# Kernel optimization log

Measured on AMD Instinct MI355X. Metric: run time of the kernel, lower is better.

## Reference

```python
import jax, jax.numpy as jnp
import numpy as np

L, C, D = 8, 8192, 128          # levels, classes per level, type_embedding_dim
P, F, K, S, NF = 8, 4, 4, 4, 16384
NBASIC = 11
N = L * C


def setup_inputs() -> dict:
    rng = np.random.default_rng(0)
    key = jax.random.key(0)
    ks = jax.random.split(key, 12)

    def lvl_idx(shape):
        # class at level l may only reference classes with id < l*C (topological DAG)
        return jnp.asarray(np.stack([rng.integers(0, l * C, size=shape) for l in range(1, L)]), jnp.int32)

    s = 1.0 / np.sqrt(D)

    def gru_w(k):
        return jax.random.normal(k, (D, 3 * D), jnp.float32) * s

    inp = {
        'basic_ids': jnp.asarray(rng.integers(0, NBASIC, size=(C,)), jnp.int32),
        'prop_idx': lvl_idx((C, P)),
        'func_param_idx': lvl_idx((C, F, K)),
        'func_ret_idx': lvl_idx((C, F)),
        'super_idx': lvl_idx((C, S)),
        'glob_param_idx': jnp.asarray(rng.integers(0, N, size=(NF, K)), jnp.int32),
        'glob_ret_idx': jnp.asarray(rng.integers(0, N, size=(NF,)), jnp.int32),
        'basic_emb': jax.random.normal(ks[0], (NBASIC, D), jnp.float32) * 0.05,
        'empty_params': jax.random.normal(ks[1], (D,), jnp.float32) * 0.05,
        'empty_members': jax.random.normal(ks[2], (D,), jnp.float32) * 0.05,
        'W_fn': jax.random.normal(ks[3], (2 * D, D), jnp.float32) * s,
        'pW': gru_w(ks[4]), 'pU': gru_w(ks[5]), 'pb': jnp.zeros((2, 3 * D), jnp.float32),
        'mW': gru_w(ks[6]), 'mU': gru_w(ks[7]), 'mb': jnp.zeros((2, 3 * D), jnp.float32),
        'sW': gru_w(ks[8]), 'sU': gru_w(ks[9]), 'sb': jnp.zeros((2, 3 * D), jnp.float32),
    }
    return inp


def gru_run(xs, W, U, b):
    """Keras GRU (reset_after=True). xs: [B,T,D] -> final hidden [B,D]."""
    bi, br = b[0], b[1]
    gx = jnp.einsum('btd,de->bte', xs, W) + bi  # input projections, all steps at once

    def step(h, g):
        gh = h @ U + br
        xz, xr, xn = jnp.split(g, 3, axis=-1)
        hz, hr, hn = jnp.split(gh, 3, axis=-1)
        z = jax.nn.sigmoid(xz + hz)
        r = jax.nn.sigmoid(xr + hr)
        n = jnp.tanh(xn + r * hn)
        return z * h + (1.0 - z) * n, None

    h0 = jnp.zeros((xs.shape[0], W.shape[0]), xs.dtype)
    h, _ = jax.lax.scan(step, h0, jnp.swapaxes(gx, 0, 1))
    return h


def fn_embed(param_idx, ret_idx, table, empty_params, W_fn, pW, pU, pb):
    """get_embedding_for_function, batched. param_idx: [..., K]; ret_idx: [...]."""
    lead = param_idx.shape[:-1]
    n = int(np.prod(lead))
    pe = table[param_idx].reshape(n, K, D)                       # gather param embeddings
    seq = jnp.concatenate([jnp.broadcast_to(empty_params, (n, 1, D)), pe], axis=1)
    h = gru_run(seq, pW, pU, pb)                                 # [n, D]
    ret = table[ret_idx].reshape(n, D)
    out = jnp.concatenate([h, ret], axis=-1) @ W_fn              # [n, D]
    return out.reshape(lead + (D,))


def reference(basic_ids, prop_idx, func_param_idx, func_ret_idx, super_idx,
              glob_param_idx, glob_ret_idx, basic_emb, empty_params, empty_members,
              W_fn, pW, pU, pb, mW, mU, mb, sW, sU, sb):
    table = jnp.zeros((N, D), basic_emb.dtype)
    table = table.at[:C].set(basic_emb[basic_ids])               # level 0: basic types

    member_fns = []
    for l in range(1, L):                                        # topological levels
        fn_e = fn_embed(func_param_idx[l - 1], func_ret_idx[l - 1], table,
                        empty_params, W_fn, pW, pU, pb)          # [C, F, D]
        member_fns.append(fn_e)
        props = table[prop_idx[l - 1]]                           # [C, P, D]
        mseq = jnp.concatenate([jnp.broadcast_to(empty_members, (C, 1, D)), props, fn_e], axis=1)
        m = gru_run(mseq, mW, mU, mb)                            # [C, D]
        sseq = jnp.concatenate([table[super_idx[l - 1]], m[:, None, :]], axis=1)
        e = gru_run(sseq, sW, sU, sb)                            # [C, D]
        table = table.at[l * C:(l + 1) * C].set(e)

    glob = fn_embed(glob_param_idx, glob_ret_idx, table, empty_params, W_fn, pW, pU, pb)
    member_fn = jnp.stack(member_fns)                            # [L-1, C, F, D]
    return table, glob, member_fn
```

## Files before the change

kernel.cpp:

```cpp
#include <hip/hip_runtime.h>

#define LVL 8
#define C 8192
#define D 128
#define P 8
#define F 4
#define K 4
#define S 4
#define NF 16384
#define NTOT (LVL*C)

typedef __bf16 bf16;
typedef bf16 bf16x4 __attribute__((ext_vector_type(4)));
typedef bf16 bf16x8 __attribute__((ext_vector_type(8)));
typedef float f32x4 __attribute__((ext_vector_type(4)));

__device__ __forceinline__ f32x4 mfma16(bf16x8 a, bf16x8 b, f32x4 c) {
  return __builtin_amdgcn_mfma_f32_16x16x32_bf16(a, b, c, 0, 0, 0);
}
__device__ __forceinline__ bf16x4 b4(f32x4 v) {
  bf16x4 r; r[0]=(bf16)v[0]; r[1]=(bf16)v[1]; r[2]=(bf16)v[2]; r[3]=(bf16)v[3]; return r;
}
__device__ __forceinline__ float sigm(float x) { return __builtin_amdgcn_rcpf(1.f + __expf(-x)); }
__device__ __forceinline__ float tanh_(float x) { return 1.f - 2.f*__builtin_amdgcn_rcpf(1.f + __expf(2.f*x)); }

__device__ __forceinline__ void bar() {
  asm volatile("s_waitcnt lgkmcnt(0)\n\ts_barrier" ::: "memory");
}

__device__ __forceinline__ float ldf(const void* b, long i, int f) {
  return f ? ((const float*)b)[i] : (float)((const bf16*)b)[i];
}
__device__ __forceinline__ bf16x8 ldx8(const void* b, long i, int f) {
  if (f) {
    f32x4 a = *(const f32x4*)((const float*)b + i);
    f32x4 c = *(const f32x4*)((const float*)b + i + 4);
    bf16x8 r;
    r[0]=(bf16)a[0]; r[1]=(bf16)a[1]; r[2]=(bf16)a[2]; r[3]=(bf16)a[3];
    r[4]=(bf16)c[0]; r[5]=(bf16)c[1]; r[6]=(bf16)c[2]; r[7]=(bf16)c[3];
    return r;
  }
  return *(const bf16x8*)((const bf16*)b + i);
}
__device__ __forceinline__ f32x4 ld4f(const void* b, long i, int f) {
  if (f) return *(const f32x4*)((const float*)b + i);
  bf16x4 t = *(const bf16x4*)((const bf16*)b + i);
  f32x4 r; r[0]=(float)t[0]; r[1]=(float)t[1]; r[2]=(float)t[2]; r[3]=(float)t[3]; return r;
}
__device__ __forceinline__ void st4(void* b, long i, int f, f32x4 v) {
  if (f) *(f32x4*)((float*)b + i) = v;
  else   *(bf16x4*)((bf16*)b + i) = b4(v);
}

template<int NT, bool SKIPU>
__device__ __forceinline__ void gru_step(
    const bf16x8 (&AU)[3][4], const bf16x8 (&AW)[3][4],
    const f32x4& zb, const f32x4& rb, const f32x4& nbx, const f32x4& nbh,
    const bf16 (* __restrict__ hbuf)[136], const bf16 (* __restrict__ xbuf)[136],
    int l15, int quad, int gc,
    f32x4 (&h)[NT], bf16 (*hout)[136])
{
  f32x4 aZ[NT], aR[NT], aNx[NT], aNh[NT];
#pragma unroll
  for (int nt = 0; nt < NT; nt++) { aZ[nt]=zb; aR[nt]=rb; aNx[nt]=nbx; aNh[nt]=nbh; }
#pragma unroll
  for (int kt = 0; kt < 4; kt++) {
    bf16x8 Bh[NT], Bx[NT];
#pragma unroll
    for (int nt = 0; nt < NT; nt++) {
      if (!SKIPU) Bh[nt] = *(const bf16x8*)&hbuf[nt*16 + l15][kt*32 + quad*8];
      Bx[nt] = *(const bf16x8*)&xbuf[nt*16 + l15][kt*32 + quad*8];
    }
#pragma unroll
    for (int nt = 0; nt < NT; nt++) {
      if (!SKIPU) aZ[nt]  = mfma16(AU[0][kt], Bh[nt], aZ[nt]);
      aZ[nt]  = mfma16(AW[0][kt], Bx[nt], aZ[nt]);
      if (!SKIPU) aR[nt]  = mfma16(AU[1][kt], Bh[nt], aR[nt]);
      aR[nt]  = mfma16(AW[1][kt], Bx[nt], aR[nt]);
      if (!SKIPU) aNh[nt] = mfma16(AU[2][kt], Bh[nt], aNh[nt]);
      aNx[nt] = mfma16(AW[2][kt], Bx[nt], aNx[nt]);
    }
  }
#pragma unroll
  for (int nt = 0; nt < NT; nt++) {
    f32x4 hn = h[nt];
#pragma unroll
    for (int i = 0; i < 4; i++) {
      float z = sigm(aZ[nt][i]);
      float r = sigm(aR[nt][i]);
      float n = tanh_(aNx[nt][i] + r*aNh[nt][i]);
      hn[i] = z*hn[i] + (1.f - z)*n;
    }
    h[nt] = hn;
    *(bf16x4*)&hout[nt*16 + l15][gc] = b4(hn);
  }
}

__global__ __launch_bounds__(512, 1) void level_kernel(
    const bf16* __restrict__ pUt, const bf16* __restrict__ pWt, const float* __restrict__ b2p,
    const bf16* __restrict__ wtT,
    const bf16* __restrict__ mUt, const bf16* __restrict__ mWt, const float* __restrict__ b2m,
    const bf16* __restrict__ sUt, const bf16* __restrict__ sWt, const float* __restrict__ b2s,
    const void* __restrict__ empty_params, const void* __restrict__ empty_members,
    const void* __restrict__ tabR, int tabRf,
    const int* __restrict__ fpi, const int* __restrict__ fri,
    const int* __restrict__ ppi, const int* __restrict__ spi,
    void* __restrict__ out, long memfnEB, long tabEB,
    bf16* __restrict__ shadowW,
    const int* __restrict__ flagp, int mode)
{
  __shared__ __align__(16) bf16 hT[2][32][136];
  __shared__ __align__(16) bf16 xT[2][32][136];
  __shared__ __align__(16) bf16 feT[4][32][136];

  const int isf32 = *flagp;
  const int rf = (tabRf < 0) ? isf32 : tabRf;
  const int tid = threadIdx.x;
  const int w = tid >> 6;
  const int l15 = tid & 15;
  const int quad = (tid & 63) >> 4;
  const int gc = w*16 + quad*4;
  const int prow = tid >> 4;
  const int pc8 = (tid & 15) * 8;
  const int c0 = blockIdx.x * 32;

  bf16x8 AU[3][4], AW[3][4];
  f32x4 zb, rb, nbx, nbh;
  auto loadWB = [&](const bf16* Ut, const bf16* Wt, const float* b2) {
#pragma unroll
    for (int tr = 0; tr < 3; tr++)
#pragma unroll
      for (int kt = 0; kt < 4; kt++) {
        size_t o = (size_t)(tr*128 + w*16 + l15)*128 + kt*32 + quad*8;
        AU[tr][kt] = *(const bf16x8*)&Ut[o];
        AW[tr][kt] = *(const bf16x8*)&Wt[o];
      }
    zb  = *(const f32x4*)&b2[0*128 + gc];
    rb  = *(const f32x4*)&b2[1*128 + gc];
    nbx = *(const f32x4*)&b2[2*128 + gc];
    nbh = *(const f32x4*)&b2[3*128 + gc];
  };

  f32x4 hm[2];

  loadWB(pUt, pWt, b2p);
  bf16x8 eP = ldx8(empty_params, pc8, isf32);

  auto fnpass = [&](long s, int4 piv, int riv, int p) {
    bf16x8 pend0 = ldx8(tabR, (long)piv.x*128 + pc8, rf);
    bf16x8 retv  = ldx8(tabR, (long)riv*128 + pc8, rf);
    *(bf16x8*)&xT[0][prow][pc8] = eP;
    bar();

    f32x4 h[2];
#pragma unroll
    for (int nt = 0; nt < 2; nt++) { h[nt][0]=0.f; h[nt][1]=0.f; h[nt][2]=0.f; h[nt][3]=0.f; }
    bf16x8 pend1;
    int buf = 0;
#pragma unroll
    for (int t = 0; t < 5; t++) {
      if (t < 3) {
        int rn = (t==0) ? piv.y : (t==1) ? piv.z : piv.w;
        pend1 = ldx8(tabR, (long)rn*128 + pc8, rf);
      }
      if (t == 0)
        gru_step<2,true >(AU, AW, zb, rb, nbx, nbh,
                          (const bf16(*)[136])hT[buf], (const bf16(*)[136])xT[0],
                          l15, quad, gc, h, hT[1-buf]);
      else
        gru_step<2,false>(AU, AW, zb, rb, nbx, nbh,
                          (const bf16(*)[136])hT[buf], (const bf16(*)[136])xT[t&1],
                          l15, quad, gc, h, hT[1-buf]);
      if (t < 4) { *(bf16x8*)&xT[(t+1)&1][prow][pc8] = pend0; pend0 = pend1; }
      bar();
      buf ^= 1;
    }
    *(bf16x8*)&xT[0][prow][pc8] = retv;
    bar();

    f32x4 acc[2];
#pragma unroll
    for (int nt = 0; nt < 2; nt++) { acc[nt][0]=0.f; acc[nt][1]=0.f; acc[nt][2]=0.f; acc[nt][3]=0.f; }
#pragma unroll
    for (int kt = 0; kt < 8; kt++) {
      bf16x8 A = *(const bf16x8*)&wtT[(size_t)(w*16 + l15)*256 + kt*32 + quad*8];
#pragma unroll
      for (int nt = 0; nt < 2; nt++) {
        bf16x8 B = (kt < 4) ? *(const bf16x8*)&hT[buf][nt*16 + l15][kt*32 + quad*8]
                            : *(const bf16x8*)&xT[0][nt*16 + l15][(kt-4)*32 + quad*8];
        acc[nt] = mfma16(A, B, acc[nt]);
      }
    }
#pragma unroll
    for (int nt = 0; nt < 2; nt++) {
      long so = mode ? ((long)blockIdx.x*32 + nt*16 + l15)
                     : ((long)(c0 + nt*16 + l15)*4 + p);
      st4(out, memfnEB + so*128 + gc, isf32, acc[nt]);
      if (!mode) *(bf16x4*)&feT[p][nt*16 + l15][gc] = b4(acc[nt]);
    }
    bar();
  };

  if (mode) {
    long s = (long)blockIdx.x*32 + prow;
    int4 p0 = *(const int4*)&fpi[s*4];
    int r0 = fri[s];
    fnpass(s, p0, r0, 0);
    return;
  }
  {
    long sB = (long)(c0 + prow)*4;
    int4 p0 = *(const int4*)&fpi[(sB+0)*4];
    int4 p1 = *(const int4*)&fpi[(sB+1)*4];
    int4 p2 = *(const int4*)&fpi[(sB+2)*4];
    int4 p3 = *(const int4*)&fpi[(sB+3)*4];
    int4 rr = *(const int4*)&fri[sB];
    fnpass(sB+0, p0, rr.x, 0);
    fnpass(sB+1, p1, rr.y, 1);
    fnpass(sB+2, p2, rr.z, 2);
    fnpass(sB+3, p3, rr.w, 3);
  }

  loadWB(mUt, mWt, b2m);
  int4 ma  = *(const int4*)&ppi[(size_t)(c0 + prow)*8];
  int4 mb2 = *(const int4*)&ppi[(size_t)(c0 + prow)*8 + 4];
  bf16x8 pendB0 = ldx8(tabR, (long)ma.x*128 + pc8, rf);
  bf16x8 eM = ldx8(empty_members, pc8, isf32);
  *(bf16x8*)&xT[0][prow][pc8] = eM;
  bar();

#pragma unroll
  for (int nt = 0; nt < 2; nt++) { hm[nt][0]=0.f; hm[nt][1]=0.f; hm[nt][2]=0.f; hm[nt][3]=0.f; }
  {
    bf16x8 pendB1;
    int buf = 0;
#pragma unroll
    for (int t = 0; t < 13; t++) {
      if (t < 7) {
        int rn = (t==0)?ma.y:(t==1)?ma.z:(t==2)?ma.w:(t==3)?mb2.x:(t==4)?mb2.y:(t==5)?mb2.z:mb2.w;
        pendB1 = ldx8(tabR, (long)rn*128 + pc8, rf);
      }
      const bf16 (*xb)[136] = (t < 9) ? (const bf16(*)[136])xT[t&1]
                                      : (const bf16(*)[136])feT[t-9];
      if (t == 0)
        gru_step<2,true >(AU, AW, zb, rb, nbx, nbh,
                          (const bf16(*)[136])hT[buf], xb, l15, quad, gc, hm, hT[1-buf]);
      else
        gru_step<2,false>(AU, AW, zb, rb, nbx, nbh,
                          (const bf16(*)[136])hT[buf], xb, l15, quad, gc, hm, hT[1-buf]);
      if (t < 8) { *(bf16x8*)&xT[(t+1)&1][prow][pc8] = pendB0; pendB0 = pendB1; }
      bar();
      buf ^= 1;
    }
  }

  loadWB(sUt, sWt, b2s);
  int4 sa = *(const int4*)&spi[(size_t)(c0 + prow)*4];
  bf16x8 x0v    = ldx8(tabR, (long)sa.x*128 + pc8, rf);
  bf16x8 pendC0 = ldx8(tabR, (long)sa.y*128 + pc8, rf);
  *(bf16x8*)&xT[0][prow][pc8] = x0v;
  bar();

  f32x4 hs[2];
#pragma unroll
  for (int nt = 0; nt < 2; nt++) { hs[nt][0]=0.f; hs[nt][1]=0.f; hs[nt][2]=0.f; hs[nt][3]=0.f; }
  {
    bf16x8 pendC1;
    int buf = 0;
#pragma unroll
    for (int t = 0; t < 5; t++) {
      if (t < 2) {
        int rn = (t==0) ? sa.z : sa.w;
        pendC1 = ldx8(tabR, (long)rn*128 + pc8, rf);
      }
      if (t == 0)
        gru_step<2,true >(AU, AW, zb, rb, nbx, nbh,
                          (const bf16(*)[136])hT[buf], (const bf16(*)[136])xT[0],
                          l15, quad, gc, hs, hT[1-buf]);
      else
        gru_step<2,false>(AU, AW, zb, rb, nbx, nbh,
                          (const bf16(*)[136])hT[buf], (const bf16(*)[136])xT[t&1],
                          l15, quad, gc, hs, hT[1-buf]);
      if (t < 3) { *(bf16x8*)&xT[(t+1)&1][prow][pc8] = pendC0; pendC0 = pendC1; }
      else if (t == 3) {
#pragma unroll
        for (int nt = 0; nt < 2; nt++) *(bf16x4*)&xT[0][nt*16 + l15][gc] = b4(hm[nt]);
      }
      bar();
      buf ^= 1;
    }
  }
#pragma unroll
  for (int nt = 0; nt < 2; nt++) {
    long row = (long)(c0 + nt*16 + l15);
    st4(out, tabEB + row*128 + gc, isf32, hs[nt]);
    if (shadowW) *(bf16x4*)&shadowW[row*128 + gc] = b4(hs[nt]);
  }
}

__global__ void detect_kernel(const void* be, int* flag) {
  if (threadIdx.x == 0 && blockIdx.x == 0) {
    const unsigned short* u = (const unsigned short*)be;
    int f = 0;
    for (int i = 0; i < 128; i++) {
      unsigned e = (u[i] >> 7) & 0xFF;
      if (e >= 128) f = 1;
    }
    *flag = f;
  }
}

__global__ void convert_kernel(const void* pW, const void* pU, const void* mW, const void* mU,
                               const void* sW, const void* sU, const void* W_fn,
                               const void* pb, const void* mb, const void* sb,
                               bf16* pWt, bf16* pUt, bf16* mWt, bf16* mUt,
                               bf16* sWt, bf16* sUt, bf16* wtT,
                               float* b2p, float* b2m, float* b2s,
                               const int* flagp) {
  const int f = *flagp;
  int i = blockIdx.x*256 + threadIdx.x;
  const int TT = 384*128;
  if (i < 6*TT) {
    int which = i / TT, j = i - which*TT;
    int c = j >> 7, k = j & 127;
    const void* src = (which==0)?pW:(which==1)?pU:(which==2)?mW:(which==3)?mU:(which==4)?sW:sU;
    bf16* dst = (which==0)?pWt:(which==1)?pUt:(which==2)?mWt:(which==3)?mUt:(which==4)?sWt:sUt;
    dst[c*128 + k] = (bf16)ldf(src, (long)k*384 + c, f);
    return;
  }
  i -= 6*TT;
  if (i < 128*256) { int c = i >> 8, k = i & 255; wtT[c*256 + k] = (bf16)ldf(W_fn, (long)k*128 + c, f); return; }
  i -= 128*256;
  if (i < 3*512) {
    int which = i >> 9, j = i & 511;
    const void* b = (which==0)?pb:(which==1)?mb:sb;
    float* dst = (which==0)?b2p:(which==1)?b2m:b2s;
    int g = j >> 7, cc = j & 127;
    float v;
    if (g == 0)      v = ldf(b, cc, f)       + ldf(b, 384 + cc, f);
    else if (g == 1) v = ldf(b, 128 + cc, f) + ldf(b, 512 + cc, f);
    else if (g == 2) v = ldf(b, 256 + cc, f);
    else             v = ldf(b, 640 + cc, f);
    dst[j] = v;
  }
}

__global__ void level0_kernel(const int* __restrict__ basic_ids, const void* basic_emb,
                              void* out, bf16* __restrict__ shadow,
                              const int* __restrict__ flagp) {
  const int f = *flagp;
  int i = blockIdx.x*256 + threadIdx.x;
  int row = i >> 5, c4 = (i & 31) * 4;
  f32x4 v = ld4f(basic_emb, (long)basic_ids[row]*128 + c4, f);
  st4(out, (long)row*128 + c4, f, v);
  if (shadow) *(bf16x4*)&shadow[(long)row*128 + c4] = b4(v);
}

extern "C" void kernel_launch(void* const* d_in, const int* in_sizes, int n_in,
                              void* d_out, int out_size, void* d_ws, size_t ws_size,
                              hipStream_t stream) {
  const int* basic_ids      = (const int*)d_in[0];
  const int* prop_idx       = (const int*)d_in[1];
  const int* func_param_idx = (const int*)d_in[2];
  const int* func_ret_idx   = (const int*)d_in[3];
  const int* super_idx      = (const int*)d_in[4];
  const int* glob_param_idx = (const int*)d_in[5];
  const int* glob_ret_idx   = (const int*)d_in[6];
  const void* basic_emb     = d_in[7];
  const void* empty_params  = d_in[8];
  const void* empty_members = d_in[9];
  const void* W_fn = d_in[10];
  const void* pW = d_in[11]; const void* pU = d_in[12]; const void* pb = d_in[13];
  const void* mW = d_in[14]; const void* mU = d_in[15]; const void* mb = d_in[16];
  const void* sW = d_in[17]; const void* sU = d_in[18]; const void* sb = d_in[19];

  const long GB = (long)NTOT*128;
  const long MB0 = GB + (long)NF*128;
  auto FEB = [&](int l) { return MB0 + (long)(l-1)*C*F*128; };

  char* wp = (char*)d_ws;
  auto carve = [&](size_t bytes) { char* p = wp; wp += (bytes + 255) & ~(size_t)255; return p; };
  int*  flag = (int*)carve(256);
  bf16* pWt = (bf16*)carve(384*128*2);
  bf16* pUt = (bf16*)carve(384*128*2);
  bf16* mWt = (bf16*)carve(384*128*2);
  bf16* mUt = (bf16*)carve(384*128*2);
  bf16* sWt = (bf16*)carve(384*128*2);
  bf16* sUt = (bf16*)carve(384*128*2);
  bf16* wtT = (bf16*)carve(128*256*2);
  float* b2p = (float*)carve(512*4);
  float* b2m = (float*)carve(512*4);
  float* b2s = (float*)carve(512*4);
  bf16* shadow = (bf16*)carve((size_t)NTOT*128*2);

  const bool useShadow = ((size_t)(wp - (char*)d_ws) <= ws_size);
  const void* tabR = useShadow ? (const void*)shadow : (const void*)d_out;
  const int tabRf  = useShadow ? 0 : -1;
  bf16* shadowL0   = useShadow ? shadow : (bf16*)nullptr;

  detect_kernel<<<1, 64, 0, stream>>>(basic_emb, flag);
  {
    int total = 6*384*128 + 128*256 + 3*512;
    convert_kernel<<<(total + 255)/256, 256, 0, stream>>>(pW, pU, mW, mU, sW, sU, W_fn,
                                                          pb, mb, sb,
                                                          pWt, pUt, mWt, mUt, sWt, sUt, wtT,
                                                          b2p, b2m, b2s, flag);
  }
  level0_kernel<<<(C*32)/256, 256, 0, stream>>>(basic_ids, basic_emb, d_out, shadowL0, flag);

  for (int l = 1; l < LVL; l++) {
    level_kernel<<<C/32, 512, 0, stream>>>(
        pUt, pWt, b2p, wtT, mUt, mWt, b2m, sUt, sWt, b2s,
        empty_params, empty_members,
        tabR, tabRf,
        func_param_idx + (size_t)(l-1)*C*F*K,
        func_ret_idx   + (size_t)(l-1)*C*F,
        prop_idx       + (size_t)(l-1)*C*P,
        super_idx      + (size_t)(l-1)*C*S,
        d_out, FEB(l), (long)l*C*128,
        useShadow ? shadow + (size_t)l*C*128 : (bf16*)nullptr,
        flag, 0);
  }

  level_kernel<<<NF/32, 512, 0, stream>>>(
      pUt, pWt, b2p, wtT, mUt, mWt, b2m, sUt, sWt, b2s,
      empty_params, empty_members,
      tabR, tabRf,
      glob_param_idx, glob_ret_idx, nullptr, nullptr,
      d_out, GB, 0, (bf16*)nullptr,
      flag, 1);
}
```

Measured before the change: 781.6 us.

## Interleave two independent function-param GRU sequences per block to hide latency

The function-embedding GRU pass now processes two independent sequences (A and B) together in each step, using separate shared-memory h/x buffers. This halves the number of serial steps and barriers, and gives the scheduler independent MFMA and elementwise work to overlap. The return-type row loads are folded into the prefetch pipeline. The global pass now covers 64 rows per block and launches half as many blocks. In exchange, register pressure and LDS use both go up, and the global launch has fewer blocks, which lowers parallelism.

Result: slower. 808.6 us (+3.5%).

```diff
diff --git a/kernel.cpp b/kernel.cpp
--- a/kernel.cpp
+++ b/kernel.cpp
@@ -52,27 +52,26 @@
   else   *(bf16x4*)((bf16*)b + i) = b4(v);
 }
 
-template<int NT, bool SKIPU>
-__device__ __forceinline__ void gru_step(
+template<bool SKIPU>
+__device__ __forceinline__ void gru_mm(
     const bf16x8 (&AU)[3][4], const bf16x8 (&AW)[3][4],
     const f32x4& zb, const f32x4& rb, const f32x4& nbx, const f32x4& nbh,
     const bf16 (* __restrict__ hbuf)[136], const bf16 (* __restrict__ xbuf)[136],
-    int l15, int quad, int gc,
-    f32x4 (&h)[NT], bf16 (*hout)[136])
+    int l15, int quad,
+    f32x4 (&aZ)[2], f32x4 (&aR)[2], f32x4 (&aNx)[2], f32x4 (&aNh)[2])
 {
-  f32x4 aZ[NT], aR[NT], aNx[NT], aNh[NT];
-#pragma unroll
-  for (int nt = 0; nt < NT; nt++) { aZ[nt]=zb; aR[nt]=rb; aNx[nt]=nbx; aNh[nt]=nbh; }
+#pragma unroll
+  for (int nt = 0; nt < 2; nt++) { aZ[nt]=zb; aR[nt]=rb; aNx[nt]=nbx; aNh[nt]=nbh; }
 #pragma unroll
   for (int kt = 0; kt < 4; kt++) {
-    bf16x8 Bh[NT], Bx[NT];
-#pragma unroll
-    for (int nt = 0; nt < NT; nt++) {
+    bf16x8 Bh[2], Bx[2];
+#pragma unroll
+    for (int nt = 0; nt < 2; nt++) {
       if (!SKIPU) Bh[nt] = *(const bf16x8*)&hbuf[nt*16 + l15][kt*32 + quad*8];
       Bx[nt] = *(const bf16x8*)&xbuf[nt*16 + l15][kt*32 + quad*8];
     }
 #pragma unroll
-    for (int nt = 0; nt < NT; nt++) {
+    for (int nt = 0; nt < 2; nt++) {
       if (!SKIPU) aZ[nt]  = mfma16(AU[0][kt], Bh[nt], aZ[nt]);
       aZ[nt]  = mfma16(AW[0][kt], Bx[nt], aZ[nt]);
       if (!SKIPU) aR[nt]  = mfma16(AU[1][kt], Bh[nt], aR[nt]);
@@ -81,8 +80,14 @@
       aNx[nt] = mfma16(AW[2][kt], Bx[nt], aNx[nt]);
     }
   }
-#pragma unroll
-  for (int nt = 0; nt < NT; nt++) {
+}
+
+__device__ __forceinline__ void gru_elem(
+    const f32x4 (&aZ)[2], const f32x4 (&aR)[2], const f32x4 (&aNx)[2], const f32x4 (&aNh)[2],
+    int l15, int gc, f32x4 (&h)[2], bf16 (*hout)[136])
+{
+#pragma unroll
+  for (int nt = 0; nt < 2; nt++) {
     f32x4 hn = h[nt];
 #pragma unroll
     for (int i = 0; i < 4; i++) {
@@ -109,8 +114,10 @@
     bf16* __restrict__ shadowW,
     const int* __restrict__ flagp, int mode)
 {
-  __shared__ __align__(16) bf16 hT[2][32][136];
-  __shared__ __align__(16) bf16 xT[2][32][136];
+  __shared__ __align__(16) bf16 hTa[2][32][136];
+  __shared__ __align__(16) bf16 xTa[2][32][136];
+  __shared__ __align__(16) bf16 hTb[2][32][136];
+  __shared__ __align__(16) bf16 xTb[2][32][136];
   __shared__ __align__(16) bf16 feT[4][32][136];
 
   const int isf32 = *flagp;
@@ -146,79 +153,111 @@
   loadWB(pUt, pWt, b2p);
   bf16x8 eP = ldx8(empty_params, pc8, isf32);
 
-  auto fnpass = [&](long s, int4 piv, int riv, int p) {
-    bf16x8 pend0 = ldx8(tabR, (long)piv.x*128 + pc8, rf);
-    bf16x8 retv  = ldx8(tabR, (long)riv*128 + pc8, rf);
-    *(bf16x8*)&xT[0][prow][pc8] = eP;
+  auto fnpair = [&](int4 pivA, int4 pivB, int rivA, int rivB, int pa, int pb) {
+    bf16x8 pA0 = ldx8(tabR, (long)pivA.x*128 + pc8, rf);
+    bf16x8 pB0 = ldx8(tabR, (long)pivB.x*128 + pc8, rf);
+    *(bf16x8*)&xTa[0][prow][pc8] = eP;
+    *(bf16x8*)&xTb[0][prow][pc8] = eP;
     bar();
 
-    f32x4 h[2];
-#pragma unroll
-    for (int nt = 0; nt < 2; nt++) { h[nt][0]=0.f; h[nt][1]=0.f; h[nt][2]=0.f; h[nt][3]=0.f; }
-    bf16x8 pend1;
+    f32x4 hA[2], hB[2];
+#pragma unroll
+    for (int nt = 0; nt < 2; nt++) {
+      hA[nt][0]=0.f; hA[nt][1]=0.f; hA[nt][2]=0.f; hA[nt][3]=0.f;
+      hB[nt][0]=0.f; hB[nt][1]=0.f; hB[nt][2]=0.f; hB[nt][3]=0.f;
+    }
+    bf16x8 pA1, pB1;
     int buf = 0;
 #pragma unroll
     for (int t = 0; t < 5; t++) {
       if (t < 3) {
-        int rn = (t==0) ? piv.y : (t==1) ? piv.z : piv.w;
-        pend1 = ldx8(tabR, (long)rn*128 + pc8, rf);
-      }
-      if (t == 0)
-        gru_step<2,true >(AU, AW, zb, rb, nbx, nbh,
-                          (const bf16(*)[136])hT[buf], (const bf16(*)[136])xT[0],
-                          l15, quad, gc, h, hT[1-buf]);
-      else
-        gru_step<2,false>(AU, AW, zb, rb, nbx, nbh,
-                          (const bf16(*)[136])hT[buf], (const bf16(*)[136])xT[t&1],
-                          l15, quad, gc, h, hT[1-buf]);
-      if (t < 4) { *(bf16x8*)&xT[(t+1)&1][prow][pc8] = pend0; pend0 = pend1; }
+        int rnA = (t==0) ? pivA.y : (t==1) ? pivA.z : pivA.w;
+        int rnB = (t==0) ? pivB.y : (t==1) ? pivB.z : pivB.w;
+        pA1 = ldx8(tabR, (long)rnA*128 + pc8, rf);
+        pB1 = ldx8(tabR, (long)rnB*128 + pc8, rf);
+      } else if (t == 3) {
+        pA1 = ldx8(tabR, (long)rivA*128 + pc8, rf);
+        pB1 = ldx8(tabR, (long)rivB*128 + pc8, rf);
+      }
+      f32x4 aZA[2], aRA[2], aNxA[2], aNhA[2];
+      f32x4 aZB[2], aRB[2], aNxB[2], aNhB[2];
+      if (t == 0) {
+        gru_mm<true >(AU,AW,zb,rb,nbx,nbh,(const bf16(*)[136])hTa[buf],(const bf16(*)[136])xTa[0],l15,quad,aZA,aRA,aNxA,aNhA);
+        gru_mm<true >(AU,AW,zb,rb,nbx,nbh,(const bf16(*)[136])hTb[buf],(const bf16(*)[136])xTb[0],l15,quad,aZB,aRB,aNxB,aNhB);
+      } else {
+        gru_mm<false>(AU,AW,zb,rb,nbx,nbh,(const bf16(*)[136])hTa[buf],(const bf16(*)[136])xTa[t&1],l15,quad,aZA,aRA,aNxA,aNhA);
+        gru_mm<false>(AU,AW,zb,rb,nbx,nbh,(const bf16(*)[136])hTb[buf],(const bf16(*)[136])xTb[t&1],l15,quad,aZB,aRB,aNxB,aNhB);
+      }
+      gru_elem(aZA,aRA,aNxA,aNhA,l15,gc,hA,hTa[1-buf]);
+      gru_elem(aZB,aRB,aNxB,aNhB,l15,gc,hB,hTb[1-buf]);
+      if (t < 4) {
+        *(bf16x8*)&xTa[(t+1)&1][prow][pc8] = pA0; pA0 = pA1;
+        *(bf16x8*)&xTb[(t+1)&1][prow][pc8] = pB0; pB0 = pB1;
+      }
       bar();
       buf ^= 1;
     }
-    *(bf16x8*)&xT[0][prow][pc8] = retv;
+    *(bf16x8*)&xTa[0][prow][pc8] = pA0;
+    *(bf16x8*)&xTb[0][prow][pc8] = pB0;
     bar();
 
-    f32x4 acc[2];
-#pragma unroll
-    for (int nt = 0; nt < 2; nt++) { acc[nt][0]=0.f; acc[nt][1]=0.f; acc[nt][2]=0.f; acc[nt][3]=0.f; }
+    f32x4 accA[2], accB[2];
+#pragma unroll
+    for (int nt = 0; nt < 2; nt++) {
+      accA[nt][0]=0.f; accA[nt][1]=0.f; accA[nt][2]=0.f; accA[nt][3]=0.f;
+      accB[nt][0]=0.f; accB[nt][1]=0.f; accB[nt][2]=0.f; accB[nt][3]=0.f;
+    }
 #pragma unroll
     for (int kt = 0; kt < 8; kt++) {
       bf16x8 A = *(const bf16x8*)&wtT[(size_t)(w*16 + l15)*256 + kt*32 + quad*8];
 #pragma unroll
       for (int nt = 0; nt < 2; nt++) {
-        bf16x8 B = (kt < 4) ? *(const bf16x8*)&hT[buf][nt*16 + l15][kt*32 + quad*8]
-                            : *(const bf16x8*)&xT[0][nt*16 + l15][(kt-4)*32 + quad*8];
-        acc[nt] = mfma16(A, B, acc[nt]);
+        bf16x8 Ba = (kt < 4) ? *(const bf16x8*)&hTa[buf][nt*16 + l15][kt*32 + quad*8]
+                             : *(const bf16x8*)&xTa[0][nt*16 + l15][(kt-4)*32 + quad*8];
+        accA[nt] = mfma16(A, Ba, accA[nt]);
+        bf16x8 Bb = (kt < 4) ? *(const bf16x8*)&hTb[buf][nt*16 + l15][kt*32 + quad*8]
+                             : *(const bf16x8*)&xTb[0][nt*16 + l15][(kt-4)*32 + quad*8];
+        accB[nt] = mfma16(A, Bb, accB[nt]);
       }
     }
 #pragma unroll
     for (int nt = 0; nt < 2; nt++) {
-      long so = mode ? ((long)blockIdx.x*32 + nt*16 + l15)
-                     : ((long)(c0 + nt*16 + l15)*4 + p);
-      st4(out, memfnEB + so*128 + gc, isf32, acc[nt]);
-      if (!mode) *(bf16x4*)&feT[p][nt*16 + l15][gc] = b4(acc[nt]);
+      long soA = mode ? ((long)blockIdx.x*64 + pa*32 + nt*16 + l15)
+                      : ((long)(c0 + nt*16 + l15)*4 + pa);
+      long soB = mode ? ((long)blockIdx.x*64 + pb*32 + nt*16 + l15)
+                      : ((long)(c0 + nt*16 + l15)*4 + pb);
+      st4(out, memfnEB + soA*128 + gc, isf32, accA[nt]);
+      st4(out, memfnEB + soB*128 + gc, isf32, accB[nt]);
+      if (!mode) {
+        *(bf16x4*)&feT[pa][nt*16 + l15][gc] = b4(accA[nt]);
+        *(bf16x4*)&feT[pb][nt*16 + l15][gc] = b4(accB[nt]);
+      }
     }
     bar();
   };
 
   if (mode) {
-    long s = (long)blockIdx.x*32 + prow;
-    int4 p0 = *(const int4*)&fpi[s*4];
-    int r0 = fri[s];
-    fnpass(s, p0, r0, 0);
+    long sA = (long)blockIdx.x*64 + prow;
+    long sB = sA + 32;
+    int4 pA = *(const int4*)&fpi[sA*4];
+    int4 pB = *(const int4*)&fpi[sB*4];
+    fnpair(pA, pB, fri[sA], fri[sB], 0, 1);
     return;
   }
   {
-    long sB = (long)(c0 + prow)*4;
-    int4 p0 = *(const int4*)&fpi[(sB+0)*4];
-    int4 p1 = *(const int4*)&fpi[(sB+1)*4];
-    int4 p2 = *(const int4*)&fpi[(sB+2)*4];
-    int4 p3 = *(const int4*)&fpi[(sB+3)*4];
-    int4 rr = *(const int4*)&fri[sB];
-    fnpass(sB+0, p0, rr.x, 0);
-    fnpass(sB+1, p1, rr.y, 1);
-    fnpass(sB+2, p2, rr.z, 2);
-    fnpass(sB+3, p3, rr.w, 3);
+    long s4 = (long)(c0 + prow)*4;
+    {
+      int4 p0 = *(const int4*)&fpi[(s4+0)*4];
+      int4 p1 = *(const int4*)&fpi[(s4+1)*4];
+      int4 rr = *(const int4*)&fri[s4];
+      fnpair(p0, p1, rr.x, rr.y, 0, 1);
+    }
+    {
+      int4 p2 = *(const int4*)&fpi[(s4+2)*4];
+      int4 p3 = *(const int4*)&fpi[(s4+3)*4];
+      int4 rr = *(const int4*)&fri[s4];
+      fnpair(p2, p3, rr.z, rr.w, 2, 3);
+    }
   }
 
   loadWB(mUt, mWt, b2m);
@@ -226,7 +265,7 @@
   int4 mb2 = *(const int4*)&ppi[(size_t)(c0 + prow)*8 + 4];
   bf16x8 pendB0 = ldx8(tabR, (long)ma.x*128 + pc8, rf);
   bf16x8 eM = ldx8(empty_members, pc8, isf32);
-  *(bf16x8*)&xT[0][prow][pc8] = eM;
+  *(bf16x8*)&xTa[0][prow][pc8] = eM;
   bar();
 
 #pragma unroll
@@ -240,15 +279,15 @@
         int rn = (t==0)?ma.y:(t==1)?ma.z:(t==2)?ma.w:(t==3)?mb2.x:(t==4)?mb2.y:(t==5)?mb2.z:mb2.w;
         pendB1 = ldx8(tabR, (long)rn*128 + pc8, rf);
       }
-      const bf16 (*xb)[136] = (t < 9) ? (const bf16(*)[136])xT[t&1]
+      const bf16 (*xb)[136] = (t < 9) ? (const bf16(*)[136])xTa[t&1]
                                       : (const bf16(*)[136])feT[t-9];
+      f32x4 aZ[2], aR[2], aNx[2], aNh[2];
       if (t == 0)
-        gru_step<2,true >(AU, AW, zb, rb, nbx, nbh,
-                          (const bf16(*)[136])hT[buf], xb, l15, quad, gc, hm, hT[1-buf]);
+        gru_mm<true >(AU,AW,zb,rb,nbx,nbh,(const bf16(*)[136])hTa[buf],xb,l15,quad,aZ,aR,aNx,aNh);
       else
-        gru_step<2,false>(AU, AW, zb, rb, nbx, nbh,
-                          (const bf16(*)[136])hT[buf], xb, l15, quad, gc, hm, hT[1-buf]);
-      if (t < 8) { *(bf16x8*)&xT[(t+1)&1][prow][pc8] = pendB0; pendB0 = pendB1; }
+        gru_mm<false>(AU,AW,zb,rb,nbx,nbh,(const bf16(*)[136])hTa[buf],xb,l15,quad,aZ,aR,aNx,aNh);
+      gru_elem(aZ,aR,aNx,aNh,l15,gc,hm,hTa[1-buf]);
+      if (t < 8) { *(bf16x8*)&xTa[(t+1)&1][prow][pc8] = pendB0; pendB0 = pendB1; }
       bar();
       buf ^= 1;
     }
@@ -258,7 +297,7 @@
   int4 sa = *(const int4*)&spi[(size_t)(c0 + prow)*4];
   bf16x8 x0v    = ldx8(tabR, (long)sa.x*128 + pc8, rf);
   bf16x8 pendC0 = ldx8(tabR, (long)sa.y*128 + pc8, rf);
-  *(bf16x8*)&xT[0][prow][pc8] = x0v;
+  *(bf16x8*)&xTa[0][prow][pc8] = x0v;
   bar();
 
   f32x4 hs[2];
@@ -273,18 +312,16 @@
         int rn = (t==0) ? sa.z : sa.w;
         pendC1 = ldx8(tabR, (long)rn*128 + pc8, rf);
       }
+      f32x4 aZ[2], aR[2], aNx[2], aNh[2];
       if (t == 0)
-        gru_step<2,true >(AU, AW, zb, rb, nbx, nbh,
-                          (const bf16(*)[136])hT[buf], (const bf16(*)[136])xT[0],
-                          l15, quad, gc, hs, hT[1-buf]);
+        gru_mm<true >(AU,AW,zb,rb,nbx,nbh,(const bf16(*)[136])hTa[buf],(const bf16(*)[136])xTa[0],l15,quad,aZ,aR,aNx,aNh);
       else
-        gru_step<2,false>(AU, AW, zb, rb, nbx, nbh,
-                          (const bf16(*)[136])hT[buf], (const bf16(*)[136])xT[t&1],
-                          l15, quad, gc, hs, hT[1-buf]);
-      if (t < 3) { *(bf16x8*)&xT[(t+1)&1][prow][pc8] = pendC0; pendC0 = pendC1; }
+        gru_mm<false>(AU,AW,zb,rb,nbx,nbh,(const bf16(*)[136])hTa[buf],(const bf16(*)[136])xTa[t&1],l15,quad,aZ,aR,aNx,aNh);
+      gru_elem(aZ,aR,aNx,aNh,l15,gc,hs,hTa[1-buf]);
+      if (t < 3) { *(bf16x8*)&xTa[(t+1)&1][prow][pc8] = pendC0; pendC0 = pendC1; }
       else if (t == 3) {
 #pragma unroll
-        for (int nt = 0; nt < 2; nt++) *(bf16x4*)&xT[0][nt*16 + l15][gc] = b4(hm[nt]);
+        for (int nt = 0; nt < 2; nt++) *(bf16x4*)&xTa[0][nt*16 + l15][gc] = b4(hm[nt]);
       }
       bar();
       buf ^= 1;
@@ -422,7 +459,7 @@
         flag, 0);
   }
 
-  level_kernel<<<NF/32, 512, 0, stream>>>(
+  level_kernel<<<NF/64, 512, 0, stream>>>(
       pUt, pWt, b2p, wtT, mUt, mWt, b2m, sUt, sWt, b2s,
       empty_params, empty_members,
       tabR, tabRf,
```

## Template level kernel on rows per block, shrink to 16 rows for occupancy

Applied to the files above, without the earlier changes.

The level kernel is templated on the number of classes per block (16 or 32). At runtime it picks 16 when the occupancy query reports at least two resident blocks per CU. Launch bounds rise from one to four blocks per CU, and gate biases move from registers into shared memory to cut register pressure. Gather loads shrink to 4-element vectors, and index loads move inside each pass. The aim is more concurrent blocks to hide gather and barrier latency, at the cost of fewer MFMA tiles per weight load and possible register spilling under the tighter bound.

After: 2.013 ms. +157.5%, slower.

```diff
diff --git a/kernel.cpp b/kernel.cpp
--- a/kernel.cpp
+++ b/kernel.cpp
@@ -31,7 +31,23 @@
 __device__ __forceinline__ float ldf(const void* b, long i, int f) {
   return f ? ((const float*)b)[i] : (float)((const bf16*)b)[i];
 }
-__device__ __forceinline__ bf16x8 ldx8(const void* b, long i, int f) {
+template<int E> struct VecT {};
+template<> struct VecT<4> { using T = bf16x4; };
+template<> struct VecT<8> { using T = bf16x8; };
+
+template<int E>
+__device__ __forceinline__ typename VecT<E>::T ldxE(const void* b, long i, int f);
+template<>
+__device__ __forceinline__ bf16x4 ldxE<4>(const void* b, long i, int f) {
+  if (f) {
+    f32x4 a = *(const f32x4*)((const float*)b + i);
+    bf16x4 r; r[0]=(bf16)a[0]; r[1]=(bf16)a[1]; r[2]=(bf16)a[2]; r[3]=(bf16)a[3];
+    return r;
+  }
+  return *(const bf16x4*)((const bf16*)b + i);
+}
+template<>
+__device__ __forceinline__ bf16x8 ldxE<8>(const void* b, long i, int f) {
   if (f) {
     f32x4 a = *(const f32x4*)((const float*)b + i);
     f32x4 c = *(const f32x4*)((const float*)b + i + 4);
@@ -55,14 +71,19 @@
 template<int NT, bool SKIPU>
 __device__ __forceinline__ void gru_step(
     const bf16x8 (&AU)[3][4], const bf16x8 (&AW)[3][4],
-    const f32x4& zb, const f32x4& rb, const f32x4& nbx, const f32x4& nbh,
+    const float (* __restrict__ bias)[128],
     const bf16 (* __restrict__ hbuf)[136], const bf16 (* __restrict__ xbuf)[136],
     int l15, int quad, int gc,
     f32x4 (&h)[NT], bf16 (*hout)[136])
 {
   f32x4 aZ[NT], aR[NT], aNx[NT], aNh[NT];
 #pragma unroll
-  for (int nt = 0; nt < NT; nt++) { aZ[nt]=zb; aR[nt]=rb; aNx[nt]=nbx; aNh[nt]=nbh; }
+  for (int nt = 0; nt < NT; nt++) {
+    aZ[nt]  = *(const f32x4*)&bias[0][gc];
+    aR[nt]  = *(const f32x4*)&bias[1][gc];
+    aNx[nt] = *(const f32x4*)&bias[2][gc];
+    aNh[nt] = *(const f32x4*)&bias[3][gc];
+  }
 #pragma unroll
   for (int kt = 0; kt < 4; kt++) {
     bf16x8 Bh[NT], Bx[NT];
@@ -96,7 +117,8 @@
   }
 }
 
-__global__ __launch_bounds__(512, 1) void level_kernel(
+template<int SEQ>
+__global__ __launch_bounds__(512, 4) void level_kernel(
     const bf16* __restrict__ pUt, const bf16* __restrict__ pWt, const float* __restrict__ b2p,
     const bf16* __restrict__ wtT,
     const bf16* __restrict__ mUt, const bf16* __restrict__ mWt, const float* __restrict__ b2m,
@@ -109,9 +131,15 @@
     bf16* __restrict__ shadowW,
     const int* __restrict__ flagp, int mode)
 {
-  __shared__ __align__(16) bf16 hT[2][32][136];
-  __shared__ __align__(16) bf16 xT[2][32][136];
-  __shared__ __align__(16) bf16 feT[4][32][136];
+  constexpr int NT  = SEQ/16;
+  constexpr int TPR = 512/SEQ;
+  constexpr int E   = SEQ/4;
+  using vec = typename VecT<E>::T;
+
+  __shared__ __align__(16) bf16 hT[2][SEQ][136];
+  __shared__ __align__(16) bf16 xT[2][SEQ][136];
+  __shared__ __align__(16) bf16 feT[4][SEQ][136];
+  __shared__ __align__(16) float biasL[4][128];
 
   const int isf32 = *flagp;
   const int rf = (tabRf < 0) ? isf32 : tabRf;
@@ -120,12 +148,12 @@
   const int l15 = tid & 15;
   const int quad = (tid & 63) >> 4;
   const int gc = w*16 + quad*4;
-  const int prow = tid >> 4;
-  const int pc8 = (tid & 15) * 8;
-  const int c0 = blockIdx.x * 32;
+  const int prow = tid / TPR;
+  const int pc = (tid % TPR) * E;
+  const int c0 = blockIdx.x * SEQ;
+  const float (*bias)[128] = (const float(*)[128])biasL;
 
   bf16x8 AU[3][4], AW[3][4];
-  f32x4 zb, rb, nbx, nbh;
   auto loadWB = [&](const bf16* Ut, const bf16* Wt, const float* b2) {
 #pragma unroll
     for (int tr = 0; tr < 3; tr++)
@@ -135,65 +163,64 @@
         AU[tr][kt] = *(const bf16x8*)&Ut[o];
         AW[tr][kt] = *(const bf16x8*)&Wt[o];
       }
-    zb  = *(const f32x4*)&b2[0*128 + gc];
-    rb  = *(const f32x4*)&b2[1*128 + gc];
-    nbx = *(const f32x4*)&b2[2*128 + gc];
-    nbh = *(const f32x4*)&b2[3*128 + gc];
+    biasL[tid >> 7][tid & 127] = b2[tid];
   };
 
-  f32x4 hm[2];
+  f32x4 hm[NT];
 
   loadWB(pUt, pWt, b2p);
-  bf16x8 eP = ldx8(empty_params, pc8, isf32);
-
-  auto fnpass = [&](long s, int4 piv, int riv, int p) {
-    bf16x8 pend0 = ldx8(tabR, (long)piv.x*128 + pc8, rf);
-    bf16x8 retv  = ldx8(tabR, (long)riv*128 + pc8, rf);
-    *(bf16x8*)&xT[0][prow][pc8] = eP;
+  vec eP = ldxE<E>(empty_params, pc, isf32);
+
+  auto fnpass = [&](int p) {
+    long s = mode ? ((long)blockIdx.x*SEQ + prow)
+                  : ((long)(c0 + prow)*4 + p);
+    int4 piv = *(const int4*)&fpi[s*4];
+    int riv = fri[s];
+    vec pend0 = ldxE<E>(tabR, (long)piv.x*128 + pc, rf);
+    vec retv  = ldxE<E>(tabR, (long)riv*128 + pc, rf);
+    *(vec*)&xT[0][prow][pc] = eP;
     bar();
 
-    f32x4 h[2];
-#pragma unroll
-    for (int nt = 0; nt < 2; nt++) { h[nt][0]=0.f; h[nt][1]=0.f; h[nt][2]=0.f; h[nt][3]=0.f; }
-    bf16x8 pend1;
+    f32x4 h[NT];
+#pragma unroll
+    for (int nt = 0; nt < NT; nt++) { h[nt][0]=0.f; h[nt][1]=0.f; h[nt][2]=0.f; h[nt][3]=0.f; }
+    vec pend1;
     int buf = 0;
 #pragma unroll
     for (int t = 0; t < 5; t++) {
       if (t < 3) {
         int rn = (t==0) ? piv.y : (t==1) ? piv.z : piv.w;
-        pend1 = ldx8(tabR, (long)rn*128 + pc8, rf);
+        pend1 = ldxE<E>(tabR, (long)rn*128 + pc, rf);
       }
       if (t == 0)
-        gru_step<2,true >(AU, AW, zb, rb, nbx, nbh,
-                          (const bf16(*)[136])hT[buf], (const bf16(*)[136])xT[0],
-                          l15, quad, gc, h, hT[1-buf]);
+        gru_step<NT,true >(AU, AW, bias, (const bf16(*)[136])hT[buf],
+                           (const bf16(*)[136])xT[0], l15, quad, gc, h, hT[1-buf]);
       else
-        gru_step<2,false>(AU, AW, zb, rb, nbx, nbh,
-                          (const bf16(*)[136])hT[buf], (const bf16(*)[136])xT[t&1],
-                          l15, quad, gc, h, hT[1-buf]);
-      if (t < 4) { *(bf16x8*)&xT[(t+1)&1][prow][pc8] = pend0; pend0 = pend1; }
+        gru_step<NT,false>(AU, AW, bias, (const bf16(*)[136])hT[buf],
+                           (const bf16(*)[136])xT[t&1], l15, quad, gc, h, hT[1-buf]);
+      if (t < 4) { *(vec*)&xT[(t+1)&1][prow][pc] = pend0; pend0 = pend1; }
       bar();
       buf ^= 1;
     }
-    *(bf16x8*)&xT[0][prow][pc8] = retv;
+    *(vec*)&xT[0][prow][pc] = retv;
     bar();
 
-    f32x4 acc[2];
-#pragma unroll
-    for (int nt = 0; nt < 2; nt++) { acc[nt][0]=0.f; acc[nt][1]=0.f; acc[nt][2]=0.f; acc[nt][3]=0.f; }
+    f32x4 acc[NT];
+#pragma unroll
+    for (int nt = 0; nt < NT; nt++) { acc[nt][0]=0.f; acc[nt][1]=0.f; acc[nt][2]=0.f; acc[nt][3]=0.f; }
 #pragma unroll
     for (int kt = 0; kt < 8; kt++) {
       bf16x8 A = *(const bf16x8*)&wtT[(size_t)(w*16 + l15)*256 + kt*32 + quad*8];
 #pragma unroll
-      for (int nt = 0; nt < 2; nt++) {
+      for (int nt = 0; nt < NT; nt++) {
         bf16x8 B = (kt < 4) ? *(const bf16x8*)&hT[buf][nt*16 + l15][kt*32 + quad*8]
                             : *(const bf16x8*)&xT[0][nt*16 + l15][(kt-4)*32 + quad*8];
         acc[nt] = mfma16(A, B, acc[nt]);
       }
     }
 #pragma unroll
-    for (int nt = 0; nt < 2; nt++) {
-      long so = mode ? ((long)blockIdx.x*32 + nt*16 + l15)
+    for (int nt = 0; nt < NT; nt++) {
+      long so = mode ? ((long)blockIdx.x*SEQ + nt*16 + l15)
                      : ((long)(c0 + nt*16 + l15)*4 + p);
       st4(out, memfnEB + so*128 + gc, isf32, acc[nt]);
       if (!mode) *(bf16x4*)&feT[p][nt*16 + l15][gc] = b4(acc[nt]);
@@ -201,54 +228,35 @@
     bar();
   };
 
-  if (mode) {
-    long s = (long)blockIdx.x*32 + prow;
-    int4 p0 = *(const int4*)&fpi[s*4];
-    int r0 = fri[s];
-    fnpass(s, p0, r0, 0);
-    return;
-  }
+  if (mode) { fnpass(0); return; }
+  fnpass(0); fnpass(1); fnpass(2); fnpass(3);
+
+  loadWB(mUt, mWt, b2m);
+  vec pendB0 = ldxE<E>(tabR, (long)ppi[(size_t)(c0 + prow)*8]*128 + pc, rf);
+  vec eM = ldxE<E>(empty_members, pc, isf32);
+  *(vec*)&xT[0][prow][pc] = eM;
+  bar();
+
+#pragma unroll
+  for (int nt = 0; nt < NT; nt++) { hm[nt][0]=0.f; hm[nt][1]=0.f; hm[nt][2]=0.f; hm[nt][3]=0.f; }
   {
-    long sB = (long)(c0 + prow)*4;
-    int4 p0 = *(const int4*)&fpi[(sB+0)*4];
-    int4 p1 = *(const int4*)&fpi[(sB+1)*4];
-    int4 p2 = *(const int4*)&fpi[(sB+2)*4];
-    int4 p3 = *(const int4*)&fpi[(sB+3)*4];
-    int4 rr = *(const int4*)&fri[sB];
-    fnpass(sB+0, p0, rr.x, 0);
-    fnpass(sB+1, p1, rr.y, 1);
-    fnpass(sB+2, p2, rr.z, 2);
-    fnpass(sB+3, p3, rr.w, 3);
-  }
-
-  loadWB(mUt, mWt, b2m);
-  int4 ma  = *(const int4*)&ppi[(size_t)(c0 + prow)*8];
-  int4 mb2 = *(const int4*)&ppi[(size_t)(c0 + prow)*8 + 4];
-  bf16x8 pendB0 = ldx8(tabR, (long)ma.x*128 + pc8, rf);
-  bf16x8 eM = ldx8(empty_members, pc8, isf32);
-  *(bf16x8*)&xT[0][prow][pc8] = eM;
-  bar();
-
-#pragma unroll
-  for (int nt = 0; nt < 2; nt++) { hm[nt][0]=0.f; hm[nt][1]=0.f; hm[nt][2]=0.f; hm[nt][3]=0.f; }
-  {
-    bf16x8 pendB1;
+    vec pendB1;
     int buf = 0;
 #pragma unroll
     for (int t = 0; t < 13; t++) {
       if (t < 7) {
-        int rn = (t==0)?ma.y:(t==1)?ma.z:(t==2)?ma.w:(t==3)?mb2.x:(t==4)?mb2.y:(t==5)?mb2.z:mb2.w;
-        pendB1 = ldx8(tabR, (long)rn*128 + pc8, rf);
+        int rn = ppi[(size_t)(c0 + prow)*8 + t + 1];
+        pendB1 = ldxE<E>(tabR, (long)rn*128 + pc, rf);
       }
       const bf16 (*xb)[136] = (t < 9) ? (const bf16(*)[136])xT[t&1]
                                       : (const bf16(*)[136])feT[t-9];
       if (t == 0)
-        gru_step<2,true >(AU, AW, zb, rb, nbx, nbh,
-                          (const bf16(*)[136])hT[buf], xb, l15, quad, gc, hm, hT[1-buf]);
+        gru_step<NT,true >(AU, AW, bias, (const bf16(*)[136])hT[buf], xb,
+                           l15, quad, gc, hm, hT[1-buf]);
       else
-        gru_step<2,false>(AU, AW, zb, rb, nbx, nbh,
-                          (const bf16(*)[136])hT[buf], xb, l15, quad, gc, hm, hT[1-buf]);
-      if (t < 8) { *(bf16x8*)&xT[(t+1)&1][prow][pc8] = pendB0; pendB0 = pendB1; }
+        gru_step<NT,false>(AU, AW, bias, (const bf16(*)[136])hT[buf], xb,
+                           l15, quad, gc, hm, hT[1-buf]);
+      if (t < 8) { *(vec*)&xT[(t+1)&1][prow][pc] = pendB0; pendB0 = pendB1; }
       bar();
       buf ^= 1;
     }
@@ -256,42 +264,40 @@
 
   loadWB(sUt, sWt, b2s);
   int4 sa = *(const int4*)&spi[(size_t)(c0 + prow)*4];
-  bf16x8 x0v    = ldx8(tabR, (long)sa.x*128 + pc8, rf);
-  bf16x8 pendC0 = ldx8(tabR, (long)sa.y*128 + pc8, rf);
-  *(bf16x8*)&xT[0][prow][pc8] = x0v;
+  vec x0v    = ldxE<E>(tabR, (long)sa.x*128 + pc, rf);
+  vec pendC0 = ldxE<E>(tabR, (long)sa.y*128 + pc, rf);
+  *(vec*)&xT[0][prow][pc] = x0v;
   bar();
 
-  f32x4 hs[2];
-#pragma unroll
-  for (int nt = 0; nt < 2; nt++) { hs[nt][0]=0.f; hs[nt][1]=0.f; hs[nt][2]=0.f; hs[nt][3]=0.f; }
+  f32x4 hs[NT];
+#pragma unroll
+  for (int nt = 0; nt < NT; nt++) { hs[nt][0]=0.f; hs[nt][1]=0.f; hs[nt][2]=0.f; hs[nt][3]=0.f; }
   {
-    bf16x8 pendC1;
+    vec pendC1;
     int buf = 0;
 #pragma unroll
     for (int t = 0; t < 5; t++) {
       if (t < 2) {
         int rn = (t==0) ? sa.z : sa.w;
-        pendC1 = ldx8(tabR, (long)rn*128 + pc8, rf);
+        pendC1 = ldxE<E>(tabR, (long)rn*128 + pc, rf);
       }
       if (t == 0)
-        gru_step<2,true >(AU, AW, zb, rb, nbx, nbh,
-                          (const bf16(*)[136])hT[buf], (const bf16(*)[136])xT[0],
-                          l15, quad, gc, hs, hT[1-buf]);
+        gru_step<NT,true >(AU, AW, bias, (const bf16(*)[136])hT[buf],
+                           (const bf16(*)[136])xT[0], l15, quad, gc, hs, hT[1-buf]);
       else
-        gru_step<2,false>(AU, AW, zb, rb, nbx, nbh,
-                          (const bf16(*)[136])hT[buf], (const bf16(*)[136])xT[t&1],
-                          l15, quad, gc, hs, hT[1-buf]);
-      if (t < 3) { *(bf16x8*)&xT[(t+1)&1][prow][pc8] = pendC0; pendC0 = pendC1; }
+        gru_step<NT,false>(AU, AW, bias, (const bf16(*)[136])hT[buf],
+                           (const bf16(*)[136])xT[t&1], l15, quad, gc, hs, hT[1-buf]);
+      if (t < 3) { *(vec*)&xT[(t+1)&1][prow][pc] = pendC0; pendC0 = pendC1; }
       else if (t == 3) {
 #pragma unroll
-        for (int nt = 0; nt < 2; nt++) *(bf16x4*)&xT[0][nt*16 + l15][gc] = b4(hm[nt]);
+        for (int nt = 0; nt < NT; nt++) *(bf16x4*)&xT[0][nt*16 + l15][gc] = b4(hm[nt]);
       }
       bar();
       buf ^= 1;
     }
   }
 #pragma unroll
-  for (int nt = 0; nt < 2; nt++) {
+  for (int nt = 0; nt < NT; nt++) {
     long row = (long)(c0 + nt*16 + l15);
     st4(out, tabEB + row*128 + gc, isf32, hs[nt]);
     if (shadowW) *(bf16x4*)&shadowW[row*128 + gc] = b4(hs[nt]);
@@ -398,6 +404,11 @@
   const int tabRf  = useShadow ? 0 : -1;
   bf16* shadowL0   = useShadow ? shadow : (bf16*)nullptr;
 
+  int nb16 = 0;
+  (void)hipOccupancyMaxActiveBlocksPerMultiprocessor(
+      &nb16, reinterpret_cast<const void*>(&level_kernel<16>), 512, 0);
+  const bool s16 = (nb16 >= 2);
+
   detect_kernel<<<1, 64, 0, stream>>>(basic_emb, flag);
   {
     int total = 6*384*128 + 128*256 + 3*512;
@@ -409,24 +420,33 @@
   level0_kernel<<<(C*32)/256, 256, 0, stream>>>(basic_ids, basic_emb, d_out, shadowL0, flag);
 
   for (int l = 1; l < LVL; l++) {
-    level_kernel<<<C/32, 512, 0, stream>>>(
+    const int* fpi = func_param_idx + (size_t)(l-1)*C*F*K;
+    const int* fri = func_ret_idx   + (size_t)(l-1)*C*F;
+    const int* ppi = prop_idx       + (size_t)(l-1)*C*P;
+    const int* spi = super_idx      + (size_t)(l-1)*C*S;
+    bf16* shw = useShadow ? shadow + (size_t)l*C*128 : (bf16*)nullptr;
+    if (s16)
+      level_kernel<16><<<C/16, 512, 0, stream>>>(
+          pUt, pWt, b2p, wtT, mUt, mWt, b2m, sUt, sWt, b2s,
+          empty_params, empty_members, tabR, tabRf,
+          fpi, fri, ppi, spi, d_out, FEB(l), (long)l*C*128, shw, flag, 0);
+    else
+      level_kernel<32><<<C/32, 512, 0, stream>>>(
+          pUt, pWt, b2p, wtT, mUt, mWt, b2m, sUt, sWt, b2s,
+          empty_params, empty_members, tabR, tabRf,
+          fpi, fri, ppi, spi, d_out, FEB(l), (long)l*C*128, shw, flag, 0);
+  }
+
+  if (s16)
+    level_kernel<16><<<NF/16, 512, 0, stream>>>(
         pUt, pWt, b2p, wtT, mUt, mWt, b2m, sUt, sWt, b2s,
-        empty_params, empty_members,
-        tabR, tabRf,
-        func_param_idx + (size_t)(l-1)*C*F*K,
-        func_ret_idx   + (size_t)(l-1)*C*F,
-        prop_idx       + (size_t)(l-1)*C*P,
-        super_idx      + (size_t)(l-1)*C*S,
-        d_out, FEB(l), (long)l*C*128,
-        useShadow ? shadow + (size_t)l*C*128 : (bf16*)nullptr,
-        flag, 0);
-  }
-
-  level_kernel<<<NF/32, 512, 0, stream>>>(
-      pUt, pWt, b2p, wtT, mUt, mWt, b2m, sUt, sWt, b2s,
-      empty_params, empty_members,
-      tabR, tabRf,
-      glob_param_idx, glob_ret_idx, nullptr, nullptr,
-      d_out, GB, 0, (bf16*)nullptr,
-      flag, 1);
-}
+        empty_params, empty_members, tabR, tabRf,
+        glob_param_idx, glob_ret_idx, nullptr, nullptr,
+        d_out, GB, 0, (bf16*)nullptr, flag, 1);
+  else
+    level_kernel<32><<<NF/32, 512, 0, stream>>>(
+        pUt, pWt, b2p, wtT, mUt, mWt, b2m, sUt, sWt, b2s,
+        empty_params, empty_members, tabR, tabRf,
+        glob_param_idx, glob_ret_idx, nullptr, nullptr,
+        d_out, GB, 0, (bf16*)nullptr, flag, 1);
+}
```
